# Optimization experiments

Measured on AMD Instinct MI355X. Metric: run time of the kernel, lower is better.

The kernel has to match this reference:

```python
import jax, jax.numpy as jnp
import numpy as np

K = 5  # filter_size (matches init_kwargs)


def _adaptive_pool_matrix(size: int, k: int) -> jnp.ndarray:
    """Row-stochastic [k, size] matrix replicating torch adaptive_avg_pool1d bins."""
    P = np.zeros((k, size), np.float32)
    for i in range(k):
        s = (i * size) // k
        e = -((-(i + 1) * size) // k)  # ceil((i+1)*size/k)
        P[i, s:e] = 1.0 / (e - s)
    return jnp.asarray(P)


def setup_inputs() -> dict:
    key = jax.random.key(0)
    k1, k2, k3 = jax.random.split(key, 3)
    B, Cin, Cout, H, W = 8, 32, 32, 256, 256
    x = jax.random.normal(k1, (B, Cin, H, W), jnp.float32)
    conv_w = jax.random.normal(k2, (Cout, Cin), jnp.float32) * (1.0 / np.sqrt(Cin))
    conv_b = jax.random.normal(k3, (Cout,), jnp.float32) * 0.01
    return {"x": x, "conv_w": conv_w, "conv_b": conv_b}


def reference(x, conv_w, conv_b):
    B, Cin, H, W = x.shape
    # 1x1 conv == channel-mixing einsum
    feat = jnp.einsum('bihw,oi->bohw', x, conv_w) + conv_b[None, :, None, None]
    C = feat.shape[1]
    # adaptive_avg_pool2d(feat, K) via static pooling matrices -> per-(b,c) KxK filter
    Ph = _adaptive_pool_matrix(H, K)
    Pw = _adaptive_pool_matrix(W, K)
    filt = jnp.einsum('kh,bchw,lw->bckl', Ph, feat, Pw)  # [B, C, K, K]
    # pad per original intent ('same' output), then grouped conv with groups=B*C
    pad = (K - 1) // 2
    if (K - 1) % 2 == 0:
        p = ((pad, pad), (pad, pad))
    else:
        p = ((pad + 1, pad), (pad + 1, pad))
    inp = feat.reshape(1, B * C, H, W)
    w = filt.reshape(B * C, 1, K, K)
    out = jax.lax.conv_general_dilated(
        inp, w, window_strides=(1, 1), padding=p,
        dimension_numbers=('NCHW', 'OIHW', 'NCHW'),
        feature_group_count=B * C)
    return out.reshape(B, C, H, W)
```

## Files before the change

kernel.cpp:

```cpp
#include <hip/hip_runtime.h>


#define CIN 32
#define COUT 32
#define HW 256
#define PLANE (HW * HW)
#define BATCH 8
#define KF 5
#define BIN 52

__global__ __launch_bounds__(256) void conv1x1_pool_kernel(const float* __restrict__ x,
                                                           const float* __restrict__ Wm,
                                                           const float* __restrict__ bias,
                                                           float* __restrict__ feat,
                                                           float* __restrict__ filt_raw) {
    int b   = blockIdx.x >> 8;
    int row = blockIdx.x & 255;
    int t   = threadIdx.x;

    __shared__ __align__(16) float lds[CIN * HW];

    const float* xb = x + (size_t)b * CIN * PLANE + row * HW;
#pragma unroll
    for (int j = 0; j < 8; ++j) {
        int idx = t + 256 * j;
        int ch  = idx >> 6;
        int c4  = (idx & 63) << 2;
        *(float4*)&lds[ch * HW + c4] = *(const float4*)(xb + (size_t)ch * PLANE + c4);
    }
    __syncthreads();

    float acc[COUT];
#pragma unroll
    for (int o = 0; o < COUT; ++o) acc[o] = bias[o];
#pragma unroll
    for (int i = 0; i < CIN; ++i) {
        float xi = lds[i * HW + t];
#pragma unroll
        for (int o = 0; o < COUT; ++o) acc[o] += Wm[o * CIN + i] * xi;
    }

    float* fb = feat + (size_t)b * COUT * PLANE + row * HW + t;
#pragma unroll
    for (int o = 0; o < COUT; ++o) fb[(size_t)o * PLANE] = acc[o];

    __syncthreads();
#pragma unroll
    for (int o = 0; o < COUT; ++o) lds[o * HW + t] = acc[o];
    __syncthreads();

    if (t < COUT * KF) {
        int o  = t / KF;
        int l  = t - o * KF;
        int sl = (l * HW) / KF;
        float s = 0.f;
        for (int w = 0; w < BIN; ++w) s += lds[o * HW + sl + w];
        float* dst = filt_raw + (size_t)(b * COUT + o) * 25 + l;
#pragma unroll
        for (int k = 0; k < KF; ++k) {
            int sk = (k * HW) / KF;
            if (row >= sk && row < sk + BIN) atomicAdd(dst + k * KF, s);
        }
    }
}

#define LROW 264
__global__ __launch_bounds__(256) void dwconv_kernel(const float* __restrict__ feat,
                                                     const float* __restrict__ filt_raw,
                                                     float* __restrict__ out) {
    int bo    = blockIdx.y;
    int strip = blockIdx.x;
    int gy0   = strip * 32;
    int t     = threadIdx.x;

    __shared__ __align__(16) float s[36 * LROW];
    __shared__ float sfilt[25];
    if (t < 25) sfilt[t] = filt_raw[bo * 25 + t] * (1.0f / (52.0f * 52.0f));
    if (t < 144) {
        int lr = t >> 2, e = t & 3;
        int ci = (e < 2) ? (2 + e) : (258 + e);
        s[lr * LROW + ci] = 0.f;
    }

    const float* fb = feat + (size_t)bo * PLANE;
#pragma unroll
    for (int j = 0; j < 9; ++j) {
        int idx = t + 256 * j;
        int lr  = idx >> 6;
        int cx  = (idx & 63) * 4;
        int gy  = gy0 - 2 + lr;
        float4 v = {0.f, 0.f, 0.f, 0.f};
        if ((unsigned)gy < (unsigned)HW) v = *(const float4*)(fb + gy * HW + cx);
        *(float4*)(&s[lr * LROW + 4 + cx]) = v;
    }
    __syncthreads();

    float fw[25];
#pragma unroll
    for (int j = 0; j < 25; ++j) fw[j] = sfilt[j];

    int c = t;
    float w0[5], w1[5], w2[5], w3[5], w4[5];
#pragma unroll
    for (int j = 0; j < 5; ++j) {
        w0[j] = s[0 * LROW + 2 + c + j];
        w1[j] = s[1 * LROW + 2 + c + j];
        w2[j] = s[2 * LROW + 2 + c + j];
        w3[j] = s[3 * LROW + 2 + c + j];
    }
    float* ob = out + (size_t)bo * PLANE + (size_t)gy0 * HW + c;
#pragma unroll
    for (int r = 0; r < 32; ++r) {
#pragma unroll
        for (int j = 0; j < 5; ++j) w4[j] = s[(r + 4) * LROW + 2 + c + j];
        float acc = 0.f;
#pragma unroll
        for (int j = 0; j < 5; ++j) {
            acc += fw[0 * 5 + j] * w0[j];
            acc += fw[1 * 5 + j] * w1[j];
            acc += fw[2 * 5 + j] * w2[j];
            acc += fw[3 * 5 + j] * w3[j];
            acc += fw[4 * 5 + j] * w4[j];
        }
        ob[r * HW] = acc;
#pragma unroll
        for (int j = 0; j < 5; ++j) {
            w0[j] = w1[j]; w1[j] = w2[j]; w2[j] = w3[j]; w3[j] = w4[j];
        }
    }
}

extern "C" void kernel_launch(void* const* d_in, const int* in_sizes, int n_in,
                              void* d_out, int out_size, void* d_ws, size_t ws_size,
                              hipStream_t stream) {
    const float* x      = (const float*)d_in[0];
    const float* conv_w = (const float*)d_in[1];
    const float* conv_b = (const float*)d_in[2];
    float* out = (float*)d_out;

    float* feat = (float*)d_ws;
    float* filt = feat + (size_t)BATCH * COUT * PLANE;

    hipMemsetAsync(filt, 0, BATCH * COUT * 25 * sizeof(float), stream);
    conv1x1_pool_kernel<<<dim3(BATCH * 256), dim3(256), 0, stream>>>(x, conv_w, conv_b, feat, filt);
    dwconv_kernel<<<dim3(8, BATCH * COUT), dim3(256), 0, stream>>>(feat, filt, out);
}
```

Measured before the change: 156.9 us.

## Load conv1x1 inputs directly to registers and retile dwconv into smaller strips

```diff
diff --git a/kernel.cpp b/kernel.cpp
--- a/kernel.cpp
+++ b/kernel.cpp
@@ -18,33 +18,30 @@
     int row = blockIdx.x & 255;
     int t   = threadIdx.x;
 
-    __shared__ __align__(16) float lds[CIN * HW];
-
-    const float* xb = x + (size_t)b * CIN * PLANE + row * HW;
-#pragma unroll
-    for (int j = 0; j < 8; ++j) {
-        int idx = t + 256 * j;
-        int ch  = idx >> 6;
-        int c4  = (idx & 63) << 2;
-        *(float4*)&lds[ch * HW + c4] = *(const float4*)(xb + (size_t)ch * PLANE + c4);
-    }
-    __syncthreads();
+    const float* xb = x + (size_t)b * CIN * PLANE + row * HW + t;
 
     float acc[COUT];
 #pragma unroll
     for (int o = 0; o < COUT; ++o) acc[o] = bias[o];
+
 #pragma unroll
-    for (int i = 0; i < CIN; ++i) {
-        float xi = lds[i * HW + t];
+    for (int ig = 0; ig < 4; ++ig) {
+        float xv[8];
 #pragma unroll
-        for (int o = 0; o < COUT; ++o) acc[o] += Wm[o * CIN + i] * xi;
+        for (int j = 0; j < 8; ++j) xv[j] = xb[(size_t)(ig * 8 + j) * PLANE];
+#pragma unroll
+        for (int o = 0; o < COUT; ++o) {
+#pragma unroll
+            for (int j = 0; j < 8; ++j)
+                acc[o] += Wm[o * CIN + ig * 8 + j] * xv[j];
+        }
     }
 
     float* fb = feat + (size_t)b * COUT * PLANE + row * HW + t;
 #pragma unroll
     for (int o = 0; o < COUT; ++o) fb[(size_t)o * PLANE] = acc[o];
 
-    __syncthreads();
+    __shared__ float lds[COUT * HW];
 #pragma unroll
     for (int o = 0; o < COUT; ++o) lds[o * HW + t] = acc[o];
     __syncthreads();
@@ -65,26 +62,27 @@
 }
 
 #define LROW 264
+#define STRIP 16
 __global__ __launch_bounds__(256) void dwconv_kernel(const float* __restrict__ feat,
                                                      const float* __restrict__ filt_raw,
                                                      float* __restrict__ out) {
     int bo    = blockIdx.y;
     int strip = blockIdx.x;
-    int gy0   = strip * 32;
+    int gy0   = strip * STRIP;
     int t     = threadIdx.x;
 
-    __shared__ __align__(16) float s[36 * LROW];
+    __shared__ __align__(16) float s[(STRIP + 4) * LROW];
     __shared__ float sfilt[25];
     if (t < 25) sfilt[t] = filt_raw[bo * 25 + t] * (1.0f / (52.0f * 52.0f));
-    if (t < 144) {
-        int lr = t >> 2, e = t & 3;
-        int ci = (e < 2) ? (2 + e) : (258 + e);
+    if (t < 160) {
+        int lr = t >> 3, e = t & 7;
+        int ci = (e < 4) ? e : (256 + e);
         s[lr * LROW + ci] = 0.f;
     }
 
     const float* fb = feat + (size_t)bo * PLANE;
 #pragma unroll
-    for (int j = 0; j < 9; ++j) {
+    for (int j = 0; j < 5; ++j) {
         int idx = t + 256 * j;
         int lr  = idx >> 6;
         int cx  = (idx & 63) * 4;
@@ -99,34 +97,48 @@
 #pragma unroll
     for (int j = 0; j < 25; ++j) fw[j] = sfilt[j];
 
-    int c = t;
-    float w0[5], w1[5], w2[5], w3[5], w4[5];
+    int cg  = t & 127;
+    int rq  = t >> 7;
+    int lr0 = rq * 8;
+    int ci0 = 2 * cg + 2;
+
+    float w[5][6];
 #pragma unroll
-    for (int j = 0; j < 5; ++j) {
-        w0[j] = s[0 * LROW + 2 + c + j];
-        w1[j] = s[1 * LROW + 2 + c + j];
-        w2[j] = s[2 * LROW + 2 + c + j];
-        w3[j] = s[3 * LROW + 2 + c + j];
+    for (int r = 0; r < 4; ++r) {
+        const float* rp = &s[(lr0 + r) * LROW + ci0];
+        float2 a = *(const float2*)(rp);
+        float2 c = *(const float2*)(rp + 2);
+        float2 e = *(const float2*)(rp + 4);
+        w[r][0] = a.x; w[r][1] = a.y; w[r][2] = c.x;
+        w[r][3] = c.y; w[r][4] = e.x; w[r][5] = e.y;
     }
-    float* ob = out + (size_t)bo * PLANE + (size_t)gy0 * HW + c;
+
+    float* ob = out + (size_t)bo * PLANE + (size_t)(gy0 + 8 * rq) * HW + 2 * cg;
 #pragma unroll
-    for (int r = 0; r < 32; ++r) {
+    for (int r = 0; r < 8; ++r) {
+        const float* rp = &s[(lr0 + r + 4) * LROW + ci0];
+        float2 a = *(const float2*)(rp);
+        float2 c = *(const float2*)(rp + 2);
+        float2 e = *(const float2*)(rp + 4);
+        w[4][0] = a.x; w[4][1] = a.y; w[4][2] = c.x;
+        w[4][3] = c.y; w[4][4] = e.x; w[4][5] = e.y;
+
+        float a0 = 0.f, a1 = 0.f;
 #pragma unroll
-        for (int j = 0; j < 5; ++j) w4[j] = s[(r + 4) * LROW + 2 + c + j];
-        float acc = 0.f;
+        for (int kh = 0; kh < 5; ++kh) {
 #pragma unroll
-        for (int j = 0; j < 5; ++j) {
-            acc += fw[0 * 5 + j] * w0[j];
-            acc += fw[1 * 5 + j] * w1[j];
-            acc += fw[2 * 5 + j] * w2[j];
-            acc += fw[3 * 5 + j] * w3[j];
-            acc += fw[4 * 5 + j] * w4[j];
+            for (int j = 0; j < 5; ++j) {
+                float wv = fw[kh * 5 + j];
+                a0 += wv * w[kh][j];
+                a1 += wv * w[kh][j + 1];
+            }
         }
-        ob[r * HW] = acc;
+        *(float2*)(ob + r * HW) = make_float2(a0, a1);
+
 #pragma unroll
-        for (int j = 0; j < 5; ++j) {
-            w0[j] = w1[j]; w1[j] = w2[j]; w2[j] = w3[j]; w3[j] = w4[j];
-        }
+        for (int kh = 0; kh < 4; ++kh)
+#pragma unroll
+            for (int j = 0; j < 6; ++j) w[kh][j] = w[kh + 1][j];
     }
 }
 
@@ -143,5 +155,5 @@
 
     hipMemsetAsync(filt, 0, BATCH * COUT * 25 * sizeof(float), stream);
     conv1x1_pool_kernel<<<dim3(BATCH * 256), dim3(256), 0, stream>>>(x, conv_w, conv_b, feat, filt);
-    dwconv_kernel<<<dim3(8, BATCH * COUT), dim3(256), 0, stream>>>(feat, filt, out);
+    dwconv_kernel<<<dim3(STRIP, BATCH * COUT), dim3(256), 0, stream>>>(feat, filt, out);
 }
```

Result: no change. 158.4 us (+1.0%).
